# Optimization experiments

Measured on AMD Instinct MI355X. Metric: run time of the kernel, lower is better.

The kernel has to match this reference:

```python
import jax, jax.numpy as jnp
import numpy as np
import math

ANCHOR_SIZES = (128.0, 256.0, 512.0)
ANCHOR_RATIOS = (0.5, 1.0, 2.0)
NMS_THRESH = 0.7
PRE_NMS_TOPK = 6000   # rpn_test_prenms_topk (module is in eval at __init__)
POST_NMS_TOPK = 300   # rpn_test_topk
MIN_SIZE = 16.0
BBOX_CLIP = math.log(1000.0 / 16.0)


def _base_anchors():
    scales = jnp.array(ANCHOR_SIZES, jnp.float32)
    ratios = jnp.array(ANCHOR_RATIOS, jnp.float32)
    h_r = jnp.sqrt(ratios)
    w_r = 1.0 / h_r
    ws = (w_r[:, None] * scales[None, :]).reshape(-1)  # [A], ratio-major
    hs = (h_r[:, None] * scales[None, :]).reshape(-1)
    return jnp.stack([-ws, -hs, ws, hs], axis=1) * 0.5  # [A,4] centered at origin


def _grid_anchors(img_hw, feat_hw):
    Hi, Wi = img_hw
    Hf, Wf = feat_hw
    sy, sx = Hi // Hf, Wi // Wf  # feature stride
    shift_x = jnp.arange(Wf, dtype=jnp.float32) * sx
    shift_y = jnp.arange(Hf, dtype=jnp.float32) * sy
    yy, xx = jnp.meshgrid(shift_y, shift_x, indexing='ij')
    shifts = jnp.stack([xx, yy, xx, yy], axis=-1).reshape(-1, 1, 4)
    # layout (H, W, A) matches permute(0,2,3,1) flattening of the heads
    return (shifts + _base_anchors()[None]).reshape(-1, 4)


def _conv(x, w, b, pad):
    y = jax.lax.conv_general_dilated(x, w, (1, 1), pad,
                                     dimension_numbers=('NCHW', 'OIHW', 'NCHW'))
    return y + b[None, :, None, None]


def _decode(deltas, anchors):
    wa = anchors[:, 2] - anchors[:, 0]
    ha = anchors[:, 3] - anchors[:, 1]
    cxa = anchors[:, 0] + 0.5 * wa
    cya = anchors[:, 1] + 0.5 * ha
    dx, dy = deltas[:, 0], deltas[:, 1]
    dw = jnp.minimum(deltas[:, 2], BBOX_CLIP)
    dh = jnp.minimum(deltas[:, 3], BBOX_CLIP)
    cx = dx * wa + cxa
    cy = dy * ha + cya
    w = jnp.exp(dw) * wa
    h = jnp.exp(dh) * ha
    return jnp.stack([cx - 0.5 * w, cy - 0.5 * h, cx + 0.5 * w, cy + 0.5 * h], axis=1)


def _pairwise_iou(a, b):
    area_a = (a[:, 2] - a[:, 0]) * (a[:, 3] - a[:, 1])
    area_b = (b[:, 2] - b[:, 0]) * (b[:, 3] - b[:, 1])
    lt = jnp.maximum(a[:, None, :2], b[None, :, :2])
    rb = jnp.minimum(a[:, None, 2:], b[None, :, 2:])
    wh = jnp.clip(rb - lt, 0.0)
    inter = wh[..., 0] * wh[..., 1]
    return inter / (area_a[:, None] + area_b[None, :] - inter)


def _nms_keep(boxes, valid, thresh):
    # boxes are already sorted by descending score; greedy suppression
    N = boxes.shape[0]
    iou = _pairwise_iou(boxes, boxes)  # [N,N]
    idx = jnp.arange(N)

    def body(i, keep):
        sup = keep[i] & (iou[i] > thresh) & (idx > i)
        return keep & jnp.logical_not(sup)

    return jax.lax.fori_loop(0, N, body, valid)


def setup_inputs() -> dict:
    key = jax.random.key(0)
    ks = jax.random.split(key, 6)
    C, Hf, Wf = 1024, 100, 100
    Hi, Wi = 1600, 1600
    A = len(ANCHOR_SIZES) * len(ANCHOR_RATIOS)  # 9
    std = 0.01  # matches torch.nn.init.normal_(std=0.01), bias=0
    return {
        'input_image': jax.random.normal(ks[0], (1, 3, Hi, Wi), jnp.float32),
        'feature_map': jax.random.normal(ks[1], (1, C, Hf, Wf), jnp.float32),
        'conv_w': jax.random.normal(ks[2], (C, C, 3, 3), jnp.float32) * std,
        'conv_b': jnp.zeros((C,), jnp.float32),
        'obj_w': jax.random.normal(ks[3], (A, C, 1, 1), jnp.float32) * std,
        'obj_b': jnp.zeros((A,), jnp.float32),
        'reg_w': jax.random.normal(ks[4], (4 * A, C, 1, 1), jnp.float32) * std,
        'reg_b': jnp.zeros((4 * A,), jnp.float32),
    }


def reference(input_image, feature_map, conv_w, conv_b, obj_w, obj_b, reg_w, reg_b):
    Hi, Wi = input_image.shape[-2:]
    Hf, Wf = feature_map.shape[-2:]
    A = obj_w.shape[0]

    feats = jax.nn.relu(_conv(feature_map, conv_w, conv_b, 'SAME'))
    obj = _conv(feats, obj_w, obj_b, 'VALID')   # [N,A,Hf,Wf]
    reg = _conv(feats, reg_w, reg_b, 'VALID')   # [N,4A,Hf,Wf]

    obj_flat = jnp.transpose(obj, (0, 2, 3, 1)).reshape(-1)                 # [N*Hf*Wf*A]
    reg_flat = jnp.transpose(reg.reshape(-1, A, 4, Hf, Wf),
                             (0, 3, 4, 1, 2)).reshape(-1, 4)                # [N*Hf*Wf*A,4]

    anchors = _grid_anchors((Hi, Wi), (Hf, Wf))
    boxes = _decode(jax.lax.stop_gradient(reg_flat), anchors)
    probs = jax.nn.sigmoid(jax.lax.stop_gradient(obj_flat))

    k = min(PRE_NMS_TOPK, probs.shape[0])
    top_p, top_i = jax.lax.top_k(probs, k)
    b = boxes[top_i]
    b = jnp.stack([jnp.clip(b[:, 0], 0.0, Wi), jnp.clip(b[:, 1], 0.0, Hi),
                   jnp.clip(b[:, 2], 0.0, Wi), jnp.clip(b[:, 3], 0.0, Hi)], axis=1)
    valid = ((b[:, 2] - b[:, 0]) >= MIN_SIZE) & ((b[:, 3] - b[:, 1]) >= MIN_SIZE)

    keep = _nms_keep(b, valid, NMS_THRESH)
    masked = jnp.where(keep, top_p, -1.0)
    final_s, fi = jax.lax.top_k(masked, POST_NMS_TOPK)
    final_b = b[fi]
    good = final_s > 0.0  # zero-pad slots beyond the NMS survivor count
    proposals = jnp.where(good[:, None], final_b, 0.0)
    scores = jnp.where(good, final_s, 0.0)
    return proposals, scores
```

## Files before the change

kernel.cpp:

```cpp
#include <hip/hip_runtime.h>
#include <stdint.h>

typedef unsigned int uint32;
typedef unsigned long long uint64;

#define NPIX      10000
#define NCH       1024
#define NANCH     90000
#define PRE_TOPK  6000
#define POST_TOPK 300
#define SORT_N    8192
#define NWORDS    94
#define SUP_ROWS  6016
#define BBOX_CLIP_F 4.135166556742356f

__device__ __forceinline__ uint64 shfl64(uint64 v, int lane) {
    int lo = __shfl((int)(uint32)v, lane);
    int hi = __shfl((int)(uint32)(v >> 32), lane);
    return ((uint64)(uint32)hi << 32) | (uint32)lo;
}

__global__ __launch_bounds__(256) void zero_out(float* __restrict__ out, int n) {
    int i = blockIdx.x * 256 + threadIdx.x;
    if (i < n) out[i] = 0.f;
}

__global__ __launch_bounds__(256) void repack_w(const float* __restrict__ w, float* __restrict__ W2) {
    int kk = blockIdx.x;
    int tile = blockIdx.y;
    int tci = (tile & 15) << 6;
    int tco = (tile >> 4) << 6;
    __shared__ float lds[64][65];
    int t = threadIdx.x;
    int c0 = t & 63;
    int r0 = t >> 6;
#pragma unroll
    for (int r = 0; r < 16; ++r) {
        int col = r0 + (r << 2);
        int ci = tci + c0;
        int co = tco + col;
        lds[col][c0] = w[((size_t)co * 1024 + ci) * 9 + kk];
    }
    __syncthreads();
#pragma unroll
    for (int r = 0; r < 16; ++r) {
        int row = r0 + (r << 2);
        int ci = tci + row;
        int co = tco + c0;
        W2[((size_t)kk * 1024 + ci) * 1024 + co] = lds[c0][row];
    }
}

__global__ __launch_bounds__(256) void conv3x3(const float* __restrict__ fm,
        const float* __restrict__ W2, const float* __restrict__ bias,
        float* __restrict__ feats) {
    const int n0 = blockIdx.x << 6;
    const int m0 = blockIdx.y << 6;
    const int t = threadIdx.x;
    __shared__ float Wt[32][68];
    __shared__ float Xt[32][68];
    const int lr = t >> 3;
    const int lc = (t & 7) << 3;
    int pyv[8], pxv[8];
#pragma unroll
    for (int j = 0; j < 8; ++j) {
        int p = n0 + lc + j;
        int y = p / 100;
        int x = p - y * 100;
        pyv[j] = (p < NPIX) ? y : -1000;
        pxv[j] = x;
    }
    const int tm = (t >> 4) << 2;
    const int tn = (t & 15) << 2;
    float acc[4][4] = {};
    for (int kk = 0; kk < 9; ++kk) {
        const int ky = kk / 3 - 1, kx = kk % 3 - 1;
        const float* W2k = W2 + (size_t)kk * 1024 * 1024 + m0 + lc;
        for (int ci0 = 0; ci0 < 1024; ci0 += 32) {
            __syncthreads();
            const float* wsrc = W2k + (size_t)(ci0 + lr) * 1024;
            float4 w0 = *(const float4*)(wsrc);
            float4 w1 = *(const float4*)(wsrc + 4);
            const float* fmc = fm + (size_t)(ci0 + lr) * NPIX;
            float xv[8];
#pragma unroll
            for (int j = 0; j < 8; ++j) {
                int yy = pyv[j] + ky;
                int xx = pxv[j] + kx;
                bool ok = (yy >= 0) & (yy < 100) & (xx >= 0) & (xx < 100);
                xv[j] = ok ? fmc[yy * 100 + xx] : 0.f;
            }
            *(float4*)&Wt[lr][lc] = w0;
            *(float4*)&Wt[lr][lc + 4] = w1;
            *(float4*)&Xt[lr][lc]     = make_float4(xv[0], xv[1], xv[2], xv[3]);
            *(float4*)&Xt[lr][lc + 4] = make_float4(xv[4], xv[5], xv[6], xv[7]);
            __syncthreads();
#pragma unroll
            for (int k = 0; k < 32; ++k) {
                const float4 wv = *(const float4*)&Wt[k][tm];
                const float4 xq = *(const float4*)&Xt[k][tn];
                float wr[4] = {wv.x, wv.y, wv.z, wv.w};
                float xr[4] = {xq.x, xq.y, xq.z, xq.w};
#pragma unroll
                for (int i = 0; i < 4; ++i)
#pragma unroll
                    for (int j = 0; j < 4; ++j)
                        acc[i][j] = fmaf(wr[i], xr[j], acc[i][j]);
            }
        }
    }
#pragma unroll
    for (int i = 0; i < 4; ++i) {
        int m = m0 + tm + i;
        float b = bias[m];
#pragma unroll
        for (int j = 0; j < 4; ++j) {
            int p = n0 + tn + j;
            if (p < NPIX) feats[(size_t)m * NPIX + p] = fmaxf(acc[i][j] + b, 0.f);
        }
    }
}

__global__ __launch_bounds__(256) void heads(const float* __restrict__ feats,
        const float* __restrict__ objw, const float* __restrict__ objb,
        const float* __restrict__ regw, const float* __restrict__ regb,
        uint32* __restrict__ keys32, float* __restrict__ regflat) {
    int p0 = blockIdx.x << 6;
    int t = threadIdx.x;
    int pl = t & 63;
    int g = t >> 6;
    __shared__ float fts[64][65];
    __shared__ float wl[48][64];
    float acc[12] = {};
    for (int c0 = 0; c0 < 1024; c0 += 64) {
        __syncthreads();
#pragma unroll
        for (int r = 0; r < 16; ++r) {
            int cc = g + (r << 2);
            int p = p0 + pl;
            fts[cc][pl] = (p < NPIX) ? feats[(size_t)(c0 + cc) * NPIX + p] : 0.f;
        }
#pragma unroll
        for (int i = 0; i < 12; ++i) {
            int flat = (i << 8) + t;
            int o = flat >> 6;
            int cc = flat & 63;
            float v = 0.f;
            if (o < 9) v = objw[o * 1024 + c0 + cc];
            else if (o < 45) v = regw[(o - 9) * 1024 + c0 + cc];
            wl[o][cc] = v;
        }
        __syncthreads();
#pragma unroll 16
        for (int cc = 0; cc < 64; ++cc) {
            float v = fts[cc][pl];
#pragma unroll
            for (int i = 0; i < 12; ++i)
                acc[i] = fmaf(v, wl[g + (i << 2)][cc], acc[i]);
        }
    }
    int p = p0 + pl;
    if (p < NPIX) {
#pragma unroll
        for (int i = 0; i < 12; ++i) {
            int o = g + (i << 2);
            if (o < 9) {
                float logit = acc[i] + objb[o];
                float prob = 1.f / (1.f + expf(-logit));
                keys32[p * 9 + o] = 0xFFFFFFFFu - __float_as_uint(prob);
            } else if (o < 45) {
                int ch = o - 9;
                float v = acc[i] + regb[ch];
                int a = ch >> 2, d = ch & 3;
                regflat[((size_t)p * 9 + a) * 4 + d] = v;
            }
        }
    }
}

__global__ __launch_bounds__(1024) void radix_select(const uint32* __restrict__ keys, uint32* __restrict__ meta) {
    __shared__ uint32 hist[256];
    __shared__ uint32 sPrefix, sK;
    int t = threadIdx.x;
    if (t == 0) { sPrefix = 0; sK = PRE_TOPK; }
    for (int pass = 0; pass < 4; ++pass) {
        int shift = 24 - pass * 8;
        uint32 kmask = pass ? (0xFFFFFFFFu << (32 - 8 * pass)) : 0u;
        if (t < 256) hist[t] = 0;
        __syncthreads();
        uint32 pref = sPrefix;
        for (int i = t; i < NANCH; i += 1024) {
            uint32 k = keys[i];
            if ((k & kmask) == pref) atomicAdd(&hist[(k >> shift) & 255], 1u);
        }
        __syncthreads();
        if (t == 0) {
            uint32 cum = 0, K = sK;
            for (int b = 0; b < 256; ++b) {
                uint32 c = hist[b];
                if (cum + c >= K) { sPrefix = pref | ((uint32)b << shift); sK = K - cum; break; }
                cum += c;
            }
        }
        __syncthreads();
    }
    if (t == 0) meta[0] = sPrefix;
}

__global__ __launch_bounds__(256) void compact_k(const uint32* __restrict__ keys, const uint32* __restrict__ meta,
        uint32* __restrict__ cnt, uint64* __restrict__ sel) {
    int i = blockIdx.x * 256 + threadIdx.x;
    if (i >= NANCH) return;
    uint32 T = meta[0];
    uint32 k = keys[i];
    if (k <= T) {
        uint32 pos = atomicAdd(cnt, 1u);
        if (pos < SORT_N) sel[pos] = ((uint64)k << 32) | (uint32)i;
    }
}

__global__ __launch_bounds__(1024) void bitonic_sort(const uint32* __restrict__ meta, const uint64* __restrict__ sel,
        uint64* __restrict__ sorted) {
    __shared__ uint64 arr[SORT_N];
    int t = threadIdx.x;
    uint32 cnt = meta[1]; if (cnt > SORT_N) cnt = SORT_N;
    for (int i = t; i < SORT_N; i += 1024) arr[i] = (i < (int)cnt) ? sel[i] : 0xFFFFFFFFFFFFFFFFull;
    __syncthreads();
    for (unsigned k = 2; k <= SORT_N; k <<= 1) {
        for (unsigned j = k >> 1; j > 0; j >>= 1) {
#pragma unroll 1
            for (int s = 0; s < SORT_N / 1024; ++s) {
                unsigned i = s * 1024 + t;
                unsigned l = i ^ j;
                if (l > i) {
                    uint64 a = arr[i], b = arr[l];
                    bool up = ((i & k) == 0);
                    if ((a > b) == up) { arr[i] = b; arr[l] = a; }
                }
            }
            __syncthreads();
        }
    }
    for (int i = t; i < PRE_TOPK; i += 1024) sorted[i] = arr[i];
}

__global__ __launch_bounds__(256) void decode_k(const uint64* __restrict__ sorted,
        const float* __restrict__ regflat,
        float4* __restrict__ boxes, float* __restrict__ probv, uint32* __restrict__ valid) {
    int i = blockIdx.x * 256 + threadIdx.x;
    if (i >= PRE_TOPK) return;
    uint64 v = sorted[i];
    uint32 idx = (uint32)v;
    uint32 key = (uint32)(v >> 32);
    float prob = __uint_as_float(0xFFFFFFFFu - key);
    int a = idx % 9;
    int p = idx / 9;
    int y = p / 100;
    int x = p - y * 100;
    const float ratios[3] = {0.5f, 1.0f, 2.0f};
    const float scales[3] = {128.f, 256.f, 512.f};
    float ratio = ratios[a / 3];
    float scale = scales[a % 3];
    float h_r = sqrtf(ratio);
    float w_r = 1.0f / h_r;
    float wsz = w_r * scale;
    float hsz = h_r * scale;
    float sx = 16.f * (float)x;
    float sy = 16.f * (float)y;
    float ax1 = sx - wsz * 0.5f;
    float ay1 = sy - hsz * 0.5f;
    float ax2 = sx + wsz * 0.5f;
    float ay2 = sy + hsz * 0.5f;
    float wa = ax2 - ax1;
    float ha = ay2 - ay1;
    float cxa = ax1 + 0.5f * wa;
    float cya = ay1 + 0.5f * ha;
    float dx = regflat[(size_t)idx * 4 + 0];
    float dy = regflat[(size_t)idx * 4 + 1];
    float dw = fminf(regflat[(size_t)idx * 4 + 2], BBOX_CLIP_F);
    float dh = fminf(regflat[(size_t)idx * 4 + 3], BBOX_CLIP_F);
    float cx = dx * wa + cxa;
    float cy = dy * ha + cya;
    float w = expf(dw) * wa;
    float h = expf(dh) * ha;
    float x1 = cx - 0.5f * w, y1 = cy - 0.5f * h, x2 = cx + 0.5f * w, y2 = cy + 0.5f * h;
    x1 = fminf(fmaxf(x1, 0.f), 1600.f);
    y1 = fminf(fmaxf(y1, 0.f), 1600.f);
    x2 = fminf(fmaxf(x2, 0.f), 1600.f);
    y2 = fminf(fmaxf(y2, 0.f), 1600.f);
    boxes[i] = make_float4(x1, y1, x2, y2);
    probv[i] = prob;
    valid[i] = (((x2 - x1) >= 16.f) & ((y2 - y1) >= 16.f)) ? 1u : 0u;
}

__global__ __launch_bounds__(64) void nms_pairs(const float4* __restrict__ boxes, uint64* __restrict__ sup) {
    int bi = blockIdx.y, bj = blockIdx.x;
    int t = threadIdx.x;
    int i = bi * 64 + t;
    if (bj < bi) { if (i < SUP_ROWS) sup[(size_t)i * NWORDS + bj] = 0; return; }
    __shared__ float4 bx[64];
    __shared__ float ab[64];
    int j0 = bj * 64;
    float4 bb = (j0 + t < PRE_TOPK) ? boxes[j0 + t] : make_float4(0, 0, 0, 0);
    bx[t] = bb;
    ab[t] = (bb.z - bb.x) * (bb.w - bb.y);
    __syncthreads();
    uint64 bits = 0;
    if (i < PRE_TOPK) {
        float4 ba = boxes[i];
        float aa = (ba.z - ba.x) * (ba.w - ba.y);
        for (int jj = 0; jj < 64; ++jj) {
            int j = j0 + jj;
            if (j > i && j < PRE_TOPK) {
                float4 bv = bx[jj];
                float ltx = fmaxf(ba.x, bv.x);
                float lty = fmaxf(ba.y, bv.y);
                float rbx = fminf(ba.z, bv.z);
                float rby = fminf(ba.w, bv.w);
                float wv = fmaxf(rbx - ltx, 0.f);
                float hv = fmaxf(rby - lty, 0.f);
                float inter = wv * hv;
                float iou = inter / (aa + ab[jj] - inter);
                if (iou > 0.7f) bits |= (1ull << jj);
            }
        }
    }
    if (i < SUP_ROWS) sup[(size_t)i * NWORDS + bj] = bits;
}

__global__ __launch_bounds__(64) void nms_scan(const uint32* __restrict__ valid, const uint64* __restrict__ sup,
        uint32* __restrict__ keeplist, uint32* __restrict__ kcount) {
    int l = threadIdx.x;
    __shared__ uint64 srow[64][95];
    uint64 r0 = 0, r1 = 0;
    for (int b = 0; b < 64; ++b) {
        int idx = l * 64 + b;
        if (idx < PRE_TOPK && valid[idx]) r0 |= (1ull << b);
    }
    if (l < NWORDS - 64) {
        int base = (64 + l) * 64;
        for (int b = 0; b < 64; ++b) {
            int idx = base + b;
            if (idx < PRE_TOPK && valid[idx]) r1 |= (1ull << b);
        }
    }
    int outc = 0;
    bool done = false;
    for (int c = 0; c < NWORDS && !done; ++c) {
        __syncthreads();
        for (int rr = 0; rr < 64; ++rr) {
            int row = c * 64 + rr;
            srow[rr][l] = sup[(size_t)row * NWORDS + l];
            if (l < NWORDS - 64) srow[rr][64 + l] = sup[(size_t)row * NWORDS + 64 + l];
        }
        __syncthreads();
        for (int ii = 0; ii < 64; ++ii) {
            int i = c * 64 + ii;
            if (i >= PRE_TOPK) break;
            uint64 kw = (c < 64) ? shfl64(r0, c) : shfl64(r1, c - 64);
            if ((kw >> ii) & 1ull) {
                if (l == 0) keeplist[outc] = (uint32)i;
                ++outc;
                if (outc >= POST_TOPK) { done = true; break; }
                r0 &= ~srow[ii][l];
                if (l < NWORDS - 64) r1 &= ~srow[ii][64 + l];
            }
        }
    }
    if (l == 0) *kcount = (uint32)outc;
}

__global__ __launch_bounds__(512) void finalize_k(const uint32* __restrict__ keeplist, const uint32* __restrict__ kcount,
        const float4* __restrict__ boxes, const float* __restrict__ probv, float* __restrict__ out) {
    int t = threadIdx.x;
    if (t < POST_TOPK) {
        uint32 kc = *kcount;
        if (t < (int)kc) {
            int i = keeplist[t];
            float4 b = boxes[i];
            out[t * 4 + 0] = b.x; out[t * 4 + 1] = b.y; out[t * 4 + 2] = b.z; out[t * 4 + 3] = b.w;
            out[1200 + t] = probv[i];
        } else {
            out[t * 4 + 0] = 0.f; out[t * 4 + 1] = 0.f; out[t * 4 + 2] = 0.f; out[t * 4 + 3] = 0.f;
            out[1200 + t] = 0.f;
        }
    }
}

extern "C" void kernel_launch(void* const* d_in, const int* in_sizes, int n_in,
                              void* d_out, int out_size, void* d_ws, size_t ws_size,
                              hipStream_t stream) {
    const float* fm = (const float*)d_in[1];
    const float* cw = (const float*)d_in[2];
    const float* cb = (const float*)d_in[3];
    const float* ow = (const float*)d_in[4];
    const float* ob = (const float*)d_in[5];
    const float* rw = (const float*)d_in[6];
    const float* rb = (const float*)d_in[7];
    float* out = (float*)d_out;

    uint8_t* base = (uint8_t*)d_ws;
    size_t off = 0;
    auto alloc = [&](size_t bytes) -> void* {
        void* p = base + off;
        off = (off + bytes + 255) & ~(size_t)255;
        return p;
    };
    float* feats    = (float*)alloc((size_t)NCH * NPIX * 4);
    uint32* meta    = (uint32*)alloc(64);
    uint32* keepl   = (uint32*)alloc(POST_TOPK * 4);
    uint32* kcount  = (uint32*)alloc(64);
    size_t ubase = off;
    float* W2       = (float*)alloc((size_t)9 * 1024 * 1024 * 4);
    size_t endA = off;
    off = ubase;
    uint32* keys    = (uint32*)alloc((size_t)NANCH * 4);
    float* regflat  = (float*)alloc((size_t)NANCH * 4 * 4);
    uint64* sel     = (uint64*)alloc((size_t)SORT_N * 8);
    uint64* sorted  = (uint64*)alloc((size_t)PRE_TOPK * 8);
    float4* boxes   = (float4*)alloc((size_t)PRE_TOPK * 16);
    float* probv    = (float*)alloc((size_t)PRE_TOPK * 4);
    uint32* validb  = (uint32*)alloc((size_t)PRE_TOPK * 4);
    uint64* sup     = (uint64*)alloc((size_t)SUP_ROWS * NWORDS * 8);
    size_t endB = off;
    size_t needed = (endA > endB) ? endA : endB;

    if (needed > ws_size) {
        zero_out<<<(out_size + 255) / 256, 256, 0, stream>>>(out, out_size);
        return;
    }

    hipMemsetAsync(meta, 0, 64, stream);

    repack_w<<<dim3(9, 256), 256, 0, stream>>>(cw, W2);
    conv3x3<<<dim3(157, 16), 256, 0, stream>>>(fm, W2, cb, feats);
    heads<<<157, 256, 0, stream>>>(feats, ow, ob, rw, rb, keys, regflat);
    radix_select<<<1, 1024, 0, stream>>>(keys, meta);
    compact_k<<<(NANCH + 255) / 256, 256, 0, stream>>>(keys, meta, meta + 1, sel);
    bitonic_sort<<<1, 1024, 0, stream>>>(meta, sel, sorted);
    decode_k<<<(PRE_TOPK + 255) / 256, 256, 0, stream>>>(sorted, regflat, boxes, probv, validb);
    nms_pairs<<<dim3(NWORDS, NWORDS), 64, 0, stream>>>(boxes, sup);
    nms_scan<<<1, 64, 0, stream>>>(validb, sup, keepl, kcount);
    finalize_k<<<1, 512, 0, stream>>>(keepl, kcount, boxes, probv, out);
}
```

Measured before the change: 4.184 ms.

## Replace im2col-style GEMM conv with spatial-tile halo conv and scalar weights

Rewrites the 3x3 conv as a direct spatial-tiled kernel: each block loads an 8x16 pixel tile plus halo for 16 input channels into LDS, and each wave computes 32 output channels for 128 pixels, with weights read as wave-uniform scalar loads. This removes the redundant per-tap gathers of the input and the weight staging through LDS. In exchange it needs 64 accumulators per thread, which raises register pressure, and it launches only 728 blocks, with wasted pixel lanes at the image borders. It also depends on weight loads going through the scalar cache.

```diff
diff --git a/kernel.cpp b/kernel.cpp
--- a/kernel.cpp
+++ b/kernel.cpp
@@ -14,6 +14,14 @@
 #define SUP_ROWS  6016
 #define BBOX_CLIP_F 4.135166556742356f
 
+#define TILE_H   8
+#define TILE_W   16
+#define HALO_H   10
+#define HALO_W   18
+#define HALO_WP  20
+#define CICHUNK  16
+#define CO_PER_WAVE 32
+
 __device__ __forceinline__ uint64 shfl64(uint64 v, int lane) {
     int lo = __shfl((int)(uint32)v, lane);
     int hi = __shfl((int)(uint32)(v >> 32), lane);
@@ -51,73 +59,63 @@
     }
 }
 
-__global__ __launch_bounds__(256) void conv3x3(const float* __restrict__ fm,
+__global__ __launch_bounds__(256) void conv_sw(const float* __restrict__ fm,
         const float* __restrict__ W2, const float* __restrict__ bias,
         float* __restrict__ feats) {
-    const int n0 = blockIdx.x << 6;
-    const int m0 = blockIdx.y << 6;
+    __shared__ float xt[CICHUNK][HALO_H][HALO_WP];
     const int t = threadIdx.x;
-    __shared__ float Wt[32][68];
-    __shared__ float Xt[32][68];
-    const int lr = t >> 3;
-    const int lc = (t & 7) << 3;
-    int pyv[8], pxv[8];
-#pragma unroll
-    for (int j = 0; j < 8; ++j) {
-        int p = n0 + lc + j;
-        int y = p / 100;
-        int x = p - y * 100;
-        pyv[j] = (p < NPIX) ? y : -1000;
-        pxv[j] = x;
-    }
-    const int tm = (t >> 4) << 2;
-    const int tn = (t & 15) << 2;
-    float acc[4][4] = {};
-    for (int kk = 0; kk < 9; ++kk) {
-        const int ky = kk / 3 - 1, kx = kk % 3 - 1;
-        const float* W2k = W2 + (size_t)kk * 1024 * 1024 + m0 + lc;
-        for (int ci0 = 0; ci0 < 1024; ci0 += 32) {
-            __syncthreads();
-            const float* wsrc = W2k + (size_t)(ci0 + lr) * 1024;
-            float4 w0 = *(const float4*)(wsrc);
-            float4 w1 = *(const float4*)(wsrc + 4);
-            const float* fmc = fm + (size_t)(ci0 + lr) * NPIX;
-            float xv[8];
-#pragma unroll
-            for (int j = 0; j < 8; ++j) {
-                int yy = pyv[j] + ky;
-                int xx = pxv[j] + kx;
-                bool ok = (yy >= 0) & (yy < 100) & (xx >= 0) & (xx < 100);
-                xv[j] = ok ? fmc[yy * 100 + xx] : 0.f;
-            }
-            *(float4*)&Wt[lr][lc] = w0;
-            *(float4*)&Wt[lr][lc + 4] = w1;
-            *(float4*)&Xt[lr][lc]     = make_float4(xv[0], xv[1], xv[2], xv[3]);
-            *(float4*)&Xt[lr][lc + 4] = make_float4(xv[4], xv[5], xv[6], xv[7]);
-            __syncthreads();
-#pragma unroll
-            for (int k = 0; k < 32; ++k) {
-                const float4 wv = *(const float4*)&Wt[k][tm];
-                const float4 xq = *(const float4*)&Xt[k][tn];
-                float wr[4] = {wv.x, wv.y, wv.z, wv.w};
-                float xr[4] = {xq.x, xq.y, xq.z, xq.w};
-#pragma unroll
-                for (int i = 0; i < 4; ++i)
-#pragma unroll
-                    for (int j = 0; j < 4; ++j)
-                        acc[i][j] = fmaf(wr[i], xr[j], acc[i][j]);
-            }
-        }
-    }
-#pragma unroll
-    for (int i = 0; i < 4; ++i) {
-        int m = m0 + tm + i;
-        float b = bias[m];
-#pragma unroll
-        for (int j = 0; j < 4; ++j) {
-            int p = n0 + tn + j;
-            if (p < NPIX) feats[(size_t)m * NPIX + p] = fmaxf(acc[i][j] + b, 0.f);
-        }
+    const int lane = t & 63;
+    const int wv = t >> 6;
+    const int tile = blockIdx.x;
+    const int tx0 = (tile % 7) * TILE_W;
+    const int ty0 = (tile / 7) * TILE_H;
+    const int co0 = __builtin_amdgcn_readfirstlane((blockIdx.y << 7) + (wv << 5));
+    const int ly = lane >> 3, lx = lane & 7;
+
+    float acc0[CO_PER_WAVE] = {};
+    float acc1[CO_PER_WAVE] = {};
+
+#pragma unroll 1
+    for (int c0 = 0; c0 < NCH; c0 += CICHUNK) {
+        __syncthreads();
+        for (int i = t; i < CICHUNK * HALO_H * HALO_W; i += 256) {
+            int ci = i / (HALO_H * HALO_W);
+            int rem = i - ci * (HALO_H * HALO_W);
+            int hy = rem / HALO_W;
+            int hx = rem - hy * HALO_W;
+            int gy = ty0 - 1 + hy;
+            int gx = tx0 - 1 + hx;
+            bool ok = (gy >= 0) & (gy < 100) & (gx >= 0) & (gx < 100);
+            xt[ci][hy][hx] = ok ? fm[(size_t)(c0 + ci) * NPIX + gy * 100 + gx] : 0.f;
+        }
+        __syncthreads();
+#pragma unroll 1
+        for (int ci = 0; ci < CICHUNK; ++ci) {
+#pragma unroll
+            for (int kk = 0; kk < 9; ++kk) {
+                const int ky = kk / 3, kx2 = kk % 3;
+                float x0v = xt[ci][ly + ky][lx + kx2];
+                float x1v = xt[ci][ly + ky][lx + 8 + kx2];
+                const float* wp = W2 + ((((size_t)kk << 10) + (size_t)(c0 + ci)) << 10) + co0;
+#pragma unroll
+                for (int c = 0; c < CO_PER_WAVE; ++c) {
+                    float wgt = wp[c];
+                    acc0[c] = fmaf(wgt, x0v, acc0[c]);
+                    acc1[c] = fmaf(wgt, x1v, acc1[c]);
+                }
+            }
+        }
+    }
+
+    const int gy = ty0 + ly;
+    const int gx0 = tx0 + lx;
+    const int gx1 = tx0 + 8 + lx;
+    const bool oky = gy < 100;
+#pragma unroll
+    for (int c = 0; c < CO_PER_WAVE; ++c) {
+        float b = bias[co0 + c];
+        if (oky && (gx0 < 100)) feats[(size_t)(co0 + c) * NPIX + gy * 100 + gx0] = fmaxf(acc0[c] + b, 0.f);
+        if (oky && (gx1 < 100)) feats[(size_t)(co0 + c) * NPIX + gy * 100 + gx1] = fmaxf(acc1[c] + b, 0.f);
     }
 }
 
@@ -433,7 +431,7 @@
     hipMemsetAsync(meta, 0, 64, stream);
 
     repack_w<<<dim3(9, 256), 256, 0, stream>>>(cw, W2);
-    conv3x3<<<dim3(157, 16), 256, 0, stream>>>(fm, W2, cb, feats);
+    conv_sw<<<dim3(91, 8), 256, 0, stream>>>(fm, W2, cb, feats);
     heads<<<157, 256, 0, stream>>>(feats, ow, ob, rw, rb, keys, regflat);
     radix_select<<<1, 1024, 0, stream>>>(keys, meta);
     compact_k<<<(NANCH + 255) / 256, 256, 0, stream>>>(keys, meta, meta + 1, sel);
```

After: 3.707 ms. -11.4%, faster.
